# Kernel optimization log

Measured on AMD Instinct MI355X. Metric: run time of the kernel, lower is better.

The kernel has to match this reference:

```python
import jax, jax.numpy as jnp
import numpy as np
import math

B, S, HID = 2, 2048, 1152
NH, NKV = 16, 4
HD = HID // NH  # 72
GROUPS = NH // NKV  # 4
ROPE_BASE = 10000.0


def setup_inputs() -> dict:
    key = jax.random.key(0)
    ks = jax.random.split(key, 5)
    hidden_states = jax.random.normal(ks[0], (B, S, HID), dtype=jnp.float32)
    # causal additive mask: 0 on/below diagonal, -1e9 above
    causal = jnp.tril(jnp.ones((S, S), dtype=jnp.bool_))
    attention_mask = jnp.where(causal, 0.0, -1e9).astype(jnp.float32)[None, None]
    scale = 0.02
    wq = jax.random.normal(ks[1], (HID, HID), dtype=jnp.float32) * scale
    wk = jax.random.normal(ks[2], (NKV * HD, HID), dtype=jnp.float32) * scale
    wv = jax.random.normal(ks[3], (NKV * HD, HID), dtype=jnp.float32) * scale
    wo = jax.random.normal(ks[4], (HID, HID), dtype=jnp.float32) * scale
    return {"hidden_states": hidden_states, "attention_mask": attention_mask,
            "wq": wq, "wk": wk, "wv": wv, "wo": wo}


def _rotate_half(x):
    x1, x2 = jnp.split(x, 2, axis=-1)
    return jnp.concatenate((-x2, x1), axis=-1)


def _rope_cos_sin(seq_len, dim, dtype):
    inv_freq = 1.0 / (ROPE_BASE ** (jnp.arange(0, dim, 2, dtype=jnp.float32) / dim))
    t = jnp.arange(seq_len, dtype=jnp.float32)
    freqs = jnp.outer(t, inv_freq)          # [S, dim/2]
    emb = jnp.concatenate((freqs, freqs), axis=-1)  # [S, dim]
    return jnp.cos(emb).astype(dtype), jnp.sin(emb).astype(dtype)


def reference(hidden_states, attention_mask, wq, wk, wv, wo):
    b, s, _ = hidden_states.shape
    # projections (nn.Linear: x @ W.T)
    q = (hidden_states @ wq.T).reshape(b, s, NH, HD).transpose(0, 2, 1, 3)    # [b,nh,s,hd]
    k = (hidden_states @ wk.T).reshape(b, s, NKV, HD).transpose(0, 2, 1, 3)   # [b,nkv,s,hd]
    v = (hidden_states @ wv.T).reshape(b, s, NKV, HD).transpose(0, 2, 1, 3)
    # RoPE
    cos, sin = _rope_cos_sin(s, HD, hidden_states.dtype)
    cos, sin = cos[None, None], sin[None, None]  # [1,1,s,hd]
    q = q * cos + _rotate_half(q) * sin
    k = k * cos + _rotate_half(k) * sin
    # expand kv heads (repeat_interleave over head dim)
    k = jnp.repeat(k, GROUPS, axis=1)  # [b,nh,s,hd]
    v = jnp.repeat(v, GROUPS, axis=1)
    scores = jnp.einsum('bhqd,bhkd->bhqk', q, k) / math.sqrt(HD)
    scores = scores + attention_mask
    attn = jax.nn.softmax(scores.astype(jnp.float32), axis=-1).astype(q.dtype)
    out = jnp.einsum('bhqk,bhkd->bhqd', attn, v)
    out = out.transpose(0, 2, 1, 3).reshape(b, s, HID)
    return out @ wo.T
```

## Files before the change

### kernel.cpp

```cpp
#include <hip/hip_runtime.h>
#include <hip/hip_bf16.h>
#include <cstddef>

#define B_   2
#define S_   2048
#define HID_ 1152
#define NH_  16
#define NKV_ 4
#define HD_  72
#define MTOT (B_ * S_)
#define KVDIM (NKV_ * HD_)

typedef float f32x4 __attribute__((ext_vector_type(4)));
typedef short bf16x8 __attribute__((ext_vector_type(8)));
typedef short s4v __attribute__((ext_vector_type(4)));

__device__ __forceinline__ float bf2f(short x) {
  unsigned int u = ((unsigned int)(unsigned short)x) << 16;
  return __builtin_bit_cast(float, u);
}
__device__ __forceinline__ short f2bf(float f) {
  unsigned int u = __builtin_bit_cast(unsigned int, f);
  u += 0x7fff + ((u >> 16) & 1);
  return (short)(u >> 16);
}

__device__ __forceinline__ float fast_exp2(float x) {
#if __has_builtin(__builtin_amdgcn_exp2f)
  return __builtin_amdgcn_exp2f(x);
#else
  return exp2f(x);
#endif
}

__device__ __forceinline__ void async16(const short* g, short* lds) {
  __builtin_amdgcn_global_load_lds((const __attribute__((address_space(1))) void*)g,
                                   (__attribute__((address_space(3))) void*)lds,
                                   16, 0, 0);
}

__global__ void k_cvt_all(const float4* __restrict__ s0, const float4* __restrict__ s1,
                          const float4* __restrict__ s2, const float4* __restrict__ s3,
                          const float4* __restrict__ s4,
                          s4v* __restrict__ d0, s4v* __restrict__ d1, s4v* __restrict__ d2,
                          s4v* __restrict__ d3, s4v* __restrict__ d4,
                          float2* __restrict__ tab, short* __restrict__ Vt,
                          int n0, int n1, int n2, int n3, int n4t) {
  int ncvt = n0 + n1 + n2 + n3 + n4t;
  int ntab = S_ * 36;
  int total = ncvt + ntab + 32768;
  for (int i = blockIdx.x * blockDim.x + threadIdx.x; i < total;
       i += gridDim.x * blockDim.x) {
    if (i < ncvt) {
      const float4* s;
      s4v* d;
      int off = i;
      bool perm = false;
      if (off < n0) { s = s0; d = d0; }
      else {
        off -= n0;
        if (off < n1) { s = s1; d = d1; perm = true; }
        else {
          off -= n1;
          if (off < n2) { s = s2; d = d2; perm = true; }
          else {
            off -= n2;
            if (off < n3) { s = s3; d = d3; }
            else { off -= n3; s = s4; d = d4; }
          }
        }
      }
      float4 v = s[off];
      s4v o = { f2bf(v.x), f2bf(v.y), f2bf(v.z), f2bf(v.w) };
      int out = off;
      if (perm) {
        int r = off / 288, k4 = off - r * 288;
        int hh = r / 72, ii = r - hh * 72;
        int pr = hh * 72 + (ii < 36 ? 2 * ii : 2 * (ii - 36) + 1);
        out = pr * 288 + k4;
      }
      d[out] = o;
    } else if (i < ncvt + ntab) {
      int idx = i - ncvt;
      int ii = idx % 36, s = idx / 36;
      float freq = powf(10000.0f, -(float)ii / 36.0f);
      float a = (float)s * freq;
      tab[idx] = make_float2(cosf(a), sinf(a));
    } else {
      int idx2 = i - ncvt - ntab;
      int t = idx2 << 2;
      int sp = t & 2047;
      int rest = t >> 11;
      int dr = rest & 7;
      int bkv = rest >> 3;
      s4v val = {};
      if (dr == 0) { val[0] = (short)0x3F80; val[1] = (short)0x3F80;
                     val[2] = (short)0x3F80; val[3] = (short)0x3F80; }
      *(s4v*)(Vt + (size_t)bkv * 163840 + (size_t)(72 + dr) * 2048 + sp) = val;
    }
  }
}

#define BM 128
#define BN 128
#define BK 32

__global__ __launch_bounds__(256) void k_gemm_qkv(const short* __restrict__ A,
                                                  const short* __restrict__ Wq,
                                                  const short* __restrict__ Wk,
                                                  const short* __restrict__ Wv,
                                                  short* __restrict__ Qo,
                                                  short* __restrict__ Ko,
                                                  short* __restrict__ Vt,
                                                  const float2* __restrict__ tab) {
  const int K = HID_, NTOT = 1728;
  __shared__ short As[BM * BK];
  __shared__ short Bs[BN * BK];
  const int tid = threadIdx.x;
  const int l = tid & 63;
  const int w = tid >> 6;
  const int bm = blockIdx.x * BM;
  const int bn = blockIdx.y * BN;
  const int wr = (w >> 1) * 64;
  const int wc = (w & 1) * 64;
  const int c15 = l & 15, g = l >> 4;
  const int r0 = tid >> 2;
  const int c0 = (tid & 3) * 8;

  f32x4 acc[4][4] = {};

  for (int k0 = 0; k0 < K; k0 += BK) {
#pragma unroll
    for (int it = 0; it < 2; ++it) {
      int ar = bm + it * 64 + r0;
      int br = bn + it * 64 + r0;
      if (br > NTOT - 1) br = NTOT - 1;
      const short* bsrc;
      if (br < 1152)      bsrc = Wq + (size_t)br * K;
      else if (br < 1440) bsrc = Wk + (size_t)(br - 1152) * K;
      else                bsrc = Wv + (size_t)(br - 1440) * K;
      async16(A + (size_t)ar * K + k0 + c0, &As[(it * 64 + r0) * BK + c0]);
      async16(bsrc + k0 + c0, &Bs[(it * 64 + r0) * BK + c0]);
    }
    __syncthreads();
    bf16x8 af[4], bfr[4];
#pragma unroll
    for (int t = 0; t < 4; ++t) {
      af[t]  = *(const bf16x8*)&As[(wr + t * 16 + c15) * BK + g * 8];
      bfr[t] = *(const bf16x8*)&Bs[(wc + t * 16 + c15) * BK + g * 8];
    }
#pragma unroll
    for (int mt = 0; mt < 4; ++mt)
#pragma unroll
      for (int nt = 0; nt < 4; ++nt)
        acc[mt][nt] = __builtin_amdgcn_mfma_f32_16x16x32_bf16(af[mt], bfr[nt], acc[mt][nt], 0, 0, 0);
    __syncthreads();
  }

#pragma unroll
  for (int mt = 0; mt < 4; ++mt)
#pragma unroll
    for (int nt = 0; nt < 4; ++nt) {
      int col = bn + wc + nt * 16 + c15;
      if (col < 1152) {
#pragma unroll
        for (int j = 0; j < 4; ++j) {
          int row = bm + wr + mt * 16 + g * 4 + j;
          Qo[(size_t)row * HID_ + col] = f2bf(acc[mt][nt][j]);
        }
      } else if (col < 1440) {
        int ch = col - 1152;
        int ii = (ch % 72) >> 1;
#pragma unroll
        for (int j = 0; j < 4; ++j) {
          int row = bm + wr + mt * 16 + g * 4 + j;
          float v = acc[mt][nt][j];
          float p = __shfl_xor(v, 1);
          float2 cs = tab[(size_t)(row & (S_ - 1)) * 36 + ii];
          float r = (c15 & 1) ? (v * cs.x + p * cs.y)
                              : (v * cs.x - p * cs.y);
          Ko[(size_t)row * KVDIM + ch] = f2bf(r);
        }
      } else if (col < NTOT) {
        int cv = col - 1440;
        int d = cv % 72, kvh = cv / 72;
        int row0 = bm + wr + mt * 16 + g * 4;
        int bkv = (row0 >> 11) * 4 + kvh;
        s4v out;
#pragma unroll
        for (int j = 0; j < 4; ++j) out[j] = f2bf(acc[mt][nt][j]);
        *(s4v*)(Vt + (size_t)bkv * 163840 + (size_t)d * 2048 + (row0 & 2047)) = out;
      }
    }
}

__global__ __launch_bounds__(256) void k_gemm_o(const short* __restrict__ A,
                                                const short* __restrict__ Bm,
                                                float* __restrict__ C,
                                                int M, int N, int K) {
  __shared__ short As[BM * BK];
  __shared__ short Bs[BN * BK];
  const int tid = threadIdx.x;
  const int l = tid & 63;
  const int w = tid >> 6;
  const int bm = blockIdx.x * BM;
  const int bn = blockIdx.y * BN;
  const int wr = (w >> 1) * 64;
  const int wc = (w & 1) * 64;
  const int c15 = l & 15, g = l >> 4;
  const int r0 = tid >> 2;
  const int c0 = (tid & 3) * 8;

  f32x4 acc[4][4] = {};

  for (int k0 = 0; k0 < K; k0 += BK) {
#pragma unroll
    for (int it = 0; it < 2; ++it) {
      int ar = bm + it * 64 + r0;
      int br = bn + it * 64 + r0;
      if (br > N - 1) br = N - 1;
      async16(A + (size_t)ar * K + k0 + c0, &As[(it * 64 + r0) * BK + c0]);
      async16(Bm + (size_t)br * K + k0 + c0, &Bs[(it * 64 + r0) * BK + c0]);
    }
    __syncthreads();
    bf16x8 af[4], bfr[4];
#pragma unroll
    for (int t = 0; t < 4; ++t) {
      af[t]  = *(const bf16x8*)&As[(wr + t * 16 + c15) * BK + g * 8];
      bfr[t] = *(const bf16x8*)&Bs[(wc + t * 16 + c15) * BK + g * 8];
    }
#pragma unroll
    for (int mt = 0; mt < 4; ++mt)
#pragma unroll
      for (int nt = 0; nt < 4; ++nt)
        acc[mt][nt] = __builtin_amdgcn_mfma_f32_16x16x32_bf16(af[mt], bfr[nt], acc[mt][nt], 0, 0, 0);
    __syncthreads();
  }

#pragma unroll
  for (int mt = 0; mt < 4; ++mt)
#pragma unroll
    for (int nt = 0; nt < 4; ++nt)
#pragma unroll
      for (int j = 0; j < 4; ++j) {
        int row = bm + wr + mt * 16 + g * 4 + j;
        int col = bn + wc + nt * 16 + c15;
        if (col < N) C[(size_t)row * N + col] = acc[mt][nt][j];
      }
}

#define QB 16
#define KT 64

__global__ __launch_bounds__(256, 2) void k_flash(const short* __restrict__ Q,
                                                  const short* __restrict__ Kg,
                                                  const short* __restrict__ Vt,
                                                  short* __restrict__ O,
                                                  const float2* __restrict__ tab) {
  const int bid = blockIdx.x;
  const int bkv = bid & 7;
  const int qt = 127 - (bid >> 3);
  const int b = bkv >> 2, kv = bkv & 3;
  const int tid = threadIdx.x;
  const int w = tid >> 6, l = tid & 63;
  const int h = kv * 4 + w;
  const int q0 = qt * QB;
  const int c15 = l & 15, g = l >> 4;

  __shared__ short lds[24064];
  short* Ks0 = lds;
  short* Ks1 = lds + 9728;
  short* Ps  = lds + 19456 + w * 1152;

  const float SCL = 0.117851130f * 1.4426950408889634f;
  const float SHIFT = 8.0f;

  const short* Qbase = Q + (size_t)(b * S_) * HID_ + h * HD_;
  const short* Kbase = Kg + (size_t)(b * S_) * KVDIM + kv * HD_;
  const short* Vbase = Vt + (size_t)bkv * 80 * S_;

  const short* gk[3];
  const short* gv[3];
  int lk[3], lv[3];
  bool vkf[3], vvf[3];
#pragma unroll
  for (int i = 0; i < 3; ++i) {
    int c = tid + 256 * i;
    vkf[i] = c < 576;
    int row = c / 9, cc = c - row * 9;
    if (row > 63) row = 63;
    gk[i] = Kbase + (size_t)row * KVDIM + cc * 8;
    lk[i] = c < 576 ? c * 8 : 0;
    int c2 = tid + 256 * i;
    vvf[i] = c2 < 640;
    int vrow = (c2 >> 3) & 127, slot = c2 & 7;
    if (vrow > 79) vrow = 79;
    gv[i] = Vbase + (size_t)vrow * S_ + ((slot ^ (vrow & 7)) << 3);
    lv[i] = c2 < 640 ? c2 * 8 : 0;
  }

  const int lane_k = c15 * 72 + g * 8;
  const short* rKa = Ks0 + lane_k;
  const short* rKb = Ks1 + lane_k;
  const int lane_v0 = 4608 + c15 * 64 + ((g ^ (c15 & 7)) << 3);
  const int lane_v1 = 4608 + c15 * 64 + (((4 + g) ^ (c15 & 7)) << 3);
  const short* rV0a = lds + lane_v0;
  const short* rV0b = lds + 9728 + lane_v0;
  const short* rV1a = lds + lane_v1;
  const short* rV1b = lds + 9728 + lane_v1;
  short* pPw = Ps + g * 288 + c15;
  const short* pPr = Ps + c15 * 72 + g * 8;

  bf16x8 qf[3];
  const bf16x8 zfrag = {0, 0, 0, 0, 0, 0, 0, 0};
  {
    int row = q0 + c15;
    const short* qrow = Qbase + (size_t)row * HID_;
    const float2* trow = tab + (size_t)row * 36;
#pragma unroll
    for (int ks = 0; ks < 3; ++ks) {
      int d0 = ks * 32 + g * 8;
      if (d0 < HD_) {
        bf16x8 raw = *(const bf16x8*)(qrow + d0);
        bf16x8 o;
#pragma unroll
        for (int e = 0; e < 8; e += 2) {
          float2 cs = trow[(d0 + e) >> 1];
          float x1 = bf2f(raw[e]), x2 = bf2f(raw[e + 1]);
          o[e]     = f2bf((x1 * cs.x - x2 * cs.y) * SCL);
          o[e + 1] = f2bf((x2 * cs.x + x1 * cs.y) * SCL);
        }
        qf[ks] = o;
      } else {
        qf[ks] = zfrag;
      }
    }
  }

  f32x4 accO[5] = {};

  const int nkt = (q0 + QB + KT - 1) / KT;
  const int nfull = (QB * qt + 1) >> 6;

  auto STAGE = [&](short* Kd, short* Vd) {
#pragma unroll
    for (int i = 0; i < 3; ++i) {
      if (vkf[i]) async16(gk[i], Kd + lk[i]);
      if (vvf[i]) async16(gv[i], Vd + lv[i]);
      gk[i] += KT * KVDIM;
      gv[i] += KT;
    }
  };

  STAGE(Ks0, lds + 4608);
  const short *rKc = rKa, *rKn = rKb;
  const short *rV0c = rV0a, *rV0n = rV0b;
  const short *rV1c = rV1a, *rV1n = rV1b;
  short *sKn = Ks1, *sVn = lds + 14336;
  short *sKc = Ks0, *sVc = lds + 4608;

  for (int kt = 0; kt < nkt; ++kt) {
    asm volatile("s_waitcnt vmcnt(0)" ::: "memory");
    __builtin_amdgcn_sched_barrier(0);
    __syncthreads();
    if (kt + 1 < nkt) STAGE(sKn, sVn);

    const int kbase = kt * KT;

    f32x4 sc[4] = {};
    __builtin_amdgcn_s_setprio(1);
#pragma unroll
    for (int ct = 0; ct < 4; ++ct)
#pragma unroll
      for (int ks = 0; ks < 3; ++ks) {
        bf16x8 kf = *(const bf16x8*)&rKc[ct * 1152 + ks * 32];
        sc[ct] = __builtin_amdgcn_mfma_f32_16x16x32_bf16(qf[ks], kf, sc[ct], 0, 0, 0);
      }
    __builtin_amdgcn_s_setprio(0);

    const int qrow = q0 + g * 4;
    if (kt >= nfull) {
#pragma unroll
      for (int ct = 0; ct < 4; ++ct) {
        int col = kbase + ct * 16 + c15;
#pragma unroll
        for (int j = 0; j < 4; ++j)
          if (col > qrow + j) sc[ct][j] = -1e30f;
      }
    }
#pragma unroll
    for (int ct = 0; ct < 4; ++ct)
#pragma unroll
      for (int j = 0; j < 4; ++j)
        sc[ct][j] = fast_exp2(sc[ct][j] - SHIFT);

#pragma unroll
    for (int ct = 0; ct < 4; ++ct)
#pragma unroll
      for (int j = 0; j < 4; ++j)
        pPw[j * 72 + ct * 16] = f2bf(sc[ct][j]);
    asm volatile("s_waitcnt lgkmcnt(0)" ::: "memory");
    __builtin_amdgcn_sched_barrier(0);
    bf16x8 pa0 = *(const bf16x8*)&pPr[0];
    bf16x8 pa1 = *(const bf16x8*)&pPr[32];

    __builtin_amdgcn_s_setprio(1);
#pragma unroll
    for (int dt = 0; dt < 5; ++dt) {
      bf16x8 vb0 = *(const bf16x8*)&rV0c[dt * 1024];
      bf16x8 vb1 = *(const bf16x8*)&rV1c[dt * 1024];
      accO[dt] = __builtin_amdgcn_mfma_f32_16x16x32_bf16(pa0, vb0, accO[dt], 0, 0, 0);
      accO[dt] = __builtin_amdgcn_mfma_f32_16x16x32_bf16(pa1, vb1, accO[dt], 0, 0, 0);
    }
    __builtin_amdgcn_s_setprio(0);

    const short* t;
    t = rKc; rKc = rKn; rKn = t;
    t = rV0c; rV0c = rV0n; rV0n = t;
    t = rV1c; rV1c = rV1n; rV1n = t;
    short* ts;
    ts = sKc; sKc = sKn; sKn = ts;
    ts = sVc; sVc = sVn; sVn = ts;
  }

  float lj[4];
#pragma unroll
  for (int j = 0; j < 4; ++j)
    lj[j] = 1.0f / __shfl(accO[4][j], (l & 48) | 8);
#pragma unroll
  for (int dt = 0; dt < 5; ++dt) {
    int d = dt * 16 + c15;
    if (d < HD_) {
#pragma unroll
      for (int j = 0; j < 4; ++j) {
        int row = q0 + g * 4 + j;
        O[(size_t)(b * S_ + row) * HID_ + h * HD_ + d] = f2bf(accO[dt][j] * lj[j]);
      }
    }
  }
}

extern "C" void kernel_launch(void* const* d_in, const int* in_sizes, int n_in,
                              void* d_out, int out_size, void* d_ws, size_t ws_size,
                              hipStream_t stream) {
  const float* hs = (const float*)d_in[0];
  const float* wq = (const float*)d_in[2];
  const float* wk = (const float*)d_in[3];
  const float* wv = (const float*)d_in[4];
  const float* wo = (const float*)d_in[5];

  char* ws = (char*)d_ws;
  short* Xb  = (short*)(ws + 0);
  short* Qb  = (short*)(ws + 9437184);
  short* Kb  = (short*)(ws + 18874368);
  short* Vt  = (short*)(ws + 23592960);
  short* Ob  = (short*)(ws + 26214400);
  short* wqb = (short*)(ws + 35651584);
  short* wkb = (short*)(ws + 38305792);
  short* wvb = (short*)(ws + 38969344);
  short* wob = (short*)(ws + 39632896);
  float2* tab = (float2*)(ws + 42287104);

  k_cvt_all<<<2048, 256, 0, stream>>>(
      (const float4*)hs, (const float4*)wq, (const float4*)wk, (const float4*)wv,
      (const float4*)wo,
      (s4v*)Xb, (s4v*)wqb, (s4v*)wkb, (s4v*)wvb, (s4v*)wob, tab, Vt,
      MTOT * HID_ / 4, HID_ * HID_ / 4, KVDIM * HID_ / 4, KVDIM * HID_ / 4,
      HID_ * HID_ / 4);

  k_gemm_qkv<<<dim3(32, 14), 256, 0, stream>>>(Xb, wqb, wkb, wvb, Qb, Kb, Vt, tab);

  k_flash<<<1024, 256, 0, stream>>>(Qb, Kb, Vt, Ob, tab);

  k_gemm_o<<<dim3(32, 9), 256, 0, stream>>>(Ob, wob, (float*)d_out, MTOT, HID_, HID_);
}
```

Baseline: 123.9 us.

## Double-buffer LDS tiles in QKV and output projection GEMMs

Both projection GEMMs now use two LDS buffers, so the async global-to-LDS copy of the next K tile is issued before the MFMA work on the current tile, and the buffers swap each iteration. Source pointers are computed once and advanced instead of being recomputed every iteration. This hides global load latency behind compute and removes one barrier per iteration, at the cost of doubling LDS use per block, which may lower occupancy.

```diff
diff --git a/kernel.cpp b/kernel.cpp
--- a/kernel.cpp
+++ b/kernel.cpp
@@ -114,8 +114,11 @@
                                                   short* __restrict__ Vt,
                                                   const float2* __restrict__ tab) {
   const int K = HID_, NTOT = 1728;
-  __shared__ short As[BM * BK];
-  __shared__ short Bs[BN * BK];
+  __shared__ short smem[16384];
+  short* As0 = smem;
+  short* Bs0 = smem + 4096;
+  short* As1 = smem + 8192;
+  short* Bs1 = smem + 12288;
   const int tid = threadIdx.x;
   const int l = tid & 63;
   const int w = tid >> 6;
@@ -127,34 +130,56 @@
   const int r0 = tid >> 2;
   const int c0 = (tid & 3) * 8;
 
+  const short* srcA[2];
+  const short* srcB[2];
+#pragma unroll
+  for (int it = 0; it < 2; ++it) {
+    int ar = bm + it * 64 + r0;
+    int br = bn + it * 64 + r0;
+    if (br > NTOT - 1) br = NTOT - 1;
+    const short* bsrc;
+    if (br < 1152)      bsrc = Wq + (size_t)br * K;
+    else if (br < 1440) bsrc = Wk + (size_t)(br - 1152) * K;
+    else                bsrc = Wv + (size_t)(br - 1440) * K;
+    srcA[it] = A + (size_t)ar * K + c0;
+    srcB[it] = bsrc + c0;
+  }
+
+  auto STAGE = [&](short* Ad, short* Bd) {
+#pragma unroll
+    for (int it = 0; it < 2; ++it) {
+      async16(srcA[it], &Ad[(it * 64 + r0) * BK + c0]);
+      async16(srcB[it], &Bd[(it * 64 + r0) * BK + c0]);
+      srcA[it] += BK;
+      srcB[it] += BK;
+    }
+  };
+
   f32x4 acc[4][4] = {};
 
+  STAGE(As0, Bs0);
+  short *Ac = As0, *Bc = Bs0, *An = As1, *Bn = Bs1;
+
   for (int k0 = 0; k0 < K; k0 += BK) {
-#pragma unroll
-    for (int it = 0; it < 2; ++it) {
-      int ar = bm + it * 64 + r0;
-      int br = bn + it * 64 + r0;
-      if (br > NTOT - 1) br = NTOT - 1;
-      const short* bsrc;
-      if (br < 1152)      bsrc = Wq + (size_t)br * K;
-      else if (br < 1440) bsrc = Wk + (size_t)(br - 1152) * K;
-      else                bsrc = Wv + (size_t)(br - 1440) * K;
-      async16(A + (size_t)ar * K + k0 + c0, &As[(it * 64 + r0) * BK + c0]);
-      async16(bsrc + k0 + c0, &Bs[(it * 64 + r0) * BK + c0]);
-    }
+    asm volatile("s_waitcnt vmcnt(0)" ::: "memory");
+    __builtin_amdgcn_sched_barrier(0);
     __syncthreads();
+    if (k0 + BK < K) STAGE(An, Bn);
+
     bf16x8 af[4], bfr[4];
 #pragma unroll
     for (int t = 0; t < 4; ++t) {
-      af[t]  = *(const bf16x8*)&As[(wr + t * 16 + c15) * BK + g * 8];
-      bfr[t] = *(const bf16x8*)&Bs[(wc + t * 16 + c15) * BK + g * 8];
+      af[t]  = *(const bf16x8*)&Ac[(wr + t * 16 + c15) * BK + g * 8];
+      bfr[t] = *(const bf16x8*)&Bc[(wc + t * 16 + c15) * BK + g * 8];
     }
 #pragma unroll
     for (int mt = 0; mt < 4; ++mt)
 #pragma unroll
       for (int nt = 0; nt < 4; ++nt)
         acc[mt][nt] = __builtin_amdgcn_mfma_f32_16x16x32_bf16(af[mt], bfr[nt], acc[mt][nt], 0, 0, 0);
-    __syncthreads();
+
+    short* t1 = Ac; Ac = An; An = t1;
+    short* t2 = Bc; Bc = Bn; Bn = t2;
   }
 
 #pragma unroll
@@ -198,8 +223,11 @@
                                                 const short* __restrict__ Bm,
                                                 float* __restrict__ C,
                                                 int M, int N, int K) {
-  __shared__ short As[BM * BK];
-  __shared__ short Bs[BN * BK];
+  __shared__ short smem[16384];
+  short* As0 = smem;
+  short* Bs0 = smem + 4096;
+  short* As1 = smem + 8192;
+  short* Bs1 = smem + 12288;
   const int tid = threadIdx.x;
   const int l = tid & 63;
   const int w = tid >> 6;
@@ -211,30 +239,52 @@
   const int r0 = tid >> 2;
   const int c0 = (tid & 3) * 8;
 
+  const short* srcA[2];
+  const short* srcB[2];
+#pragma unroll
+  for (int it = 0; it < 2; ++it) {
+    int ar = bm + it * 64 + r0;
+    int br = bn + it * 64 + r0;
+    if (br > N - 1) br = N - 1;
+    srcA[it] = A + (size_t)ar * K + c0;
+    srcB[it] = Bm + (size_t)br * K + c0;
+  }
+
+  auto STAGE = [&](short* Ad, short* Bd) {
+#pragma unroll
+    for (int it = 0; it < 2; ++it) {
+      async16(srcA[it], &Ad[(it * 64 + r0) * BK + c0]);
+      async16(srcB[it], &Bd[(it * 64 + r0) * BK + c0]);
+      srcA[it] += BK;
+      srcB[it] += BK;
+    }
+  };
+
   f32x4 acc[4][4] = {};
 
+  STAGE(As0, Bs0);
+  short *Ac = As0, *Bc = Bs0, *An = As1, *Bn = Bs1;
+
   for (int k0 = 0; k0 < K; k0 += BK) {
-#pragma unroll
-    for (int it = 0; it < 2; ++it) {
-      int ar = bm + it * 64 + r0;
-      int br = bn + it * 64 + r0;
-      if (br > N - 1) br = N - 1;
-      async16(A + (size_t)ar * K + k0 + c0, &As[(it * 64 + r0) * BK + c0]);
-      async16(Bm + (size_t)br * K + k0 + c0, &Bs[(it * 64 + r0) * BK + c0]);
-    }
+    asm volatile("s_waitcnt vmcnt(0)" ::: "memory");
+    __builtin_amdgcn_sched_barrier(0);
     __syncthreads();
+    if (k0 + BK < K) STAGE(An, Bn);
+
     bf16x8 af[4], bfr[4];
 #pragma unroll
     for (int t = 0; t < 4; ++t) {
-      af[t]  = *(const bf16x8*)&As[(wr + t * 16 + c15) * BK + g * 8];
-      bfr[t] = *(const bf16x8*)&Bs[(wc + t * 16 + c15) * BK + g * 8];
+      af[t]  = *(const bf16x8*)&Ac[(wr + t * 16 + c15) * BK + g * 8];
+      bfr[t] = *(const bf16x8*)&Bc[(wc + t * 16 + c15) * BK + g * 8];
     }
 #pragma unroll
     for (int mt = 0; mt < 4; ++mt)
 #pragma unroll
       for (int nt = 0; nt < 4; ++nt)
         acc[mt][nt] = __builtin_amdgcn_mfma_f32_16x16x32_bf16(af[mt], bfr[nt], acc[mt][nt], 0, 0, 0);
-    __syncthreads();
+
+    short* t1 = Ac; Ac = An; An = t1;
+    short* t2 = Bc; Bc = Bn; Bn = t2;
   }
 
 #pragma unroll
```

New measurement: 112.0 us. 9.6% less time.
